# Performance work log

Hardware: AMD Instinct MI355X
Metric: run time of the kernel (lower is better)

Reference implementation:

```python
import jax, jax.numpy as jnp
import numpy as np

EMBED_DIM = 1024
B, S = 4, 2048

def setup_inputs() -> dict:
    key = jax.random.key(0)
    ks = jax.random.split(key, 9)
    D = EMBED_DIM
    scale = 1.0 / np.sqrt(D)
    scale2 = 1.0 / np.sqrt(2 * D)
    return {
        "classical_state": jax.random.normal(ks[0], (B, S, D), jnp.float32),
        "quantum_state": jax.random.normal(ks[1], (B, S, D), jnp.float32),
        "Wc": jax.random.uniform(ks[2], (D, D), jnp.float32, -scale, scale),
        "bc": jax.random.uniform(ks[3], (D,), jnp.float32, -scale, scale),
        "Wq": jax.random.uniform(ks[4], (D, D), jnp.float32, -scale, scale),
        "bq": jax.random.uniform(ks[5], (D,), jnp.float32, -scale, scale),
        "Wg": jax.random.uniform(ks[6], (D, 2 * D), jnp.float32, -scale2, scale2),
        "bg": jax.random.uniform(ks[7], (D,), jnp.float32, -scale2, scale2),
        "temperature": jnp.array(1.0, jnp.float32),
    }

def reference(classical_state, quantum_state, Wc, bc, Wq, bq, Wg, bg, temperature):
    D = classical_state.shape[-1]
    c_proj = jnp.einsum('bsd,ed->bse', classical_state, Wc) + bc  # [B,S,D]
    q_proj = jnp.einsum('bsd,ed->bse', quantum_state, Wq) + bq    # [B,S,D]
    combined = jnp.concatenate([c_proj, q_proj], axis=-1)         # [B,S,2D]
    interface_state = jax.nn.sigmoid(jnp.einsum('bsf,ef->bse', combined, Wg) + bg)
    similarity = jnp.einsum('bsd,btd->bst', c_proj, q_proj) / jnp.sqrt(jnp.asarray(D, c_proj.dtype))
    attention_weights = jax.nn.softmax(similarity / temperature, axis=-1)  # [B,S,S]
    transfer_state = jnp.einsum('bst,btd->bsd', attention_weights, quantum_state)
    return classical_state + interface_state * transfer_state
```

## Files before the change

kernel.cpp:

```cpp
#include <hip/hip_runtime.h>


typedef unsigned short u16;
typedef unsigned char u8;
typedef __bf16 bf16x8 __attribute__((ext_vector_type(8)));
typedef float f32x4 __attribute__((ext_vector_type(4)));

__device__ __forceinline__ u16 f2bf(float f) {
    unsigned int x;
    __builtin_memcpy(&x, &f, 4);
    unsigned int r = x + 0x7FFFu + ((x >> 16) & 1u);
    return (u16)(r >> 16);
}
__device__ __forceinline__ float bf2f(u16 u) {
    unsigned int x = ((unsigned int)u) << 16;
    float f;
    __builtin_memcpy(&f, &x, 4);
    return f;
}
__device__ __forceinline__ u8 f2fp8(float f) {
    int p = __builtin_amdgcn_cvt_pk_fp8_f32(f, f, 0, false);
    return (u8)(p & 0xFF);
}

__device__ __forceinline__ void xcd_tile(int& tx, int& ty) {
    const int gx = gridDim.x;
    const int nwg = gx * gridDim.y;
    const int l = blockIdx.x + gx * blockIdx.y;
    const int per = nwg >> 3;
    const int swz = (l & 7) * per + (l >> 3);
    tx = swz % gx;
    ty = swz / gx;
}

#define GLOBAL_TO_LDS16(gp, lp)                                                           \
    __builtin_amdgcn_global_load_lds((const __attribute__((address_space(1))) void*)(gp), \
                                     (__attribute__((address_space(3))) void*)(lp), 16, 0, 0)

__global__ __launch_bounds__(256, 2) void gemm_proj(
    const u16* __restrict__ Ac, const u16* __restrict__ Aq, int lda,
    const u16* __restrict__ Bp, long sBz, int ldb,
    u8* __restrict__ C8, long sCz, int ldc, int K,
    const float* __restrict__ bc, const float* __restrict__ bq) {
    __shared__ __align__(16) u16 As[2][128 * 64];
    __shared__ __align__(16) u16 Bs[2][128 * 64];

    const int tid  = threadIdx.x;
    const int lane = tid & 63;
    const int wave = tid >> 6;
    const int z    = blockIdx.z;

    const u16* a = z ? Aq : Ac;
    const u16* b = Bp + (long)z * sBz;
    const float* bias = z ? bq : bc;

    int tx, ty;
    xcd_tile(tx, ty);
    const int tileM = ty * 128;
    const int tileN = tx * 128;

    const int wm  = wave >> 1;
    const int wn  = wave & 1;
    const int r16 = lane & 15;
    const int kg  = lane >> 4;

    const int srow = lane >> 3;
    const int sgc  = ((lane & 7) ^ (lane >> 3)) * 8;
    const int swb  = r16 & 7;

    auto stage = [&](int buf, int t) {
        const int k0 = t * 64;
#pragma unroll
        for (int p = 0; p < 4; p++) {
            const int rbase = p * 32 + wave * 8;
            GLOBAL_TO_LDS16(a + (long)(tileM + rbase + srow) * lda + k0 + sgc, &As[buf][rbase * 64]);
            GLOBAL_TO_LDS16(b + (long)(tileN + rbase + srow) * ldb + k0 + sgc, &Bs[buf][rbase * 64]);
        }
    };

    f32x4 acc[4][4] = {};

    const int nt = K / 64;
    stage(0, 0);
    stage(1, 1);

    for (int t = 0; t < nt; t++) {
        const int cur = t & 1;
        if (t + 1 < nt) asm volatile("s_waitcnt vmcnt(8)" ::: "memory");
        else            asm volatile("s_waitcnt vmcnt(0)" ::: "memory");
        __builtin_amdgcn_s_barrier();
        asm volatile("" ::: "memory");

        bf16x8 af[2][4], bfr[2][4];
#pragma unroll
        for (int h = 0; h < 2; h++) {
#pragma unroll
            for (int i = 0; i < 4; i++) {
                const int Ra = wm * 64 + i * 16 + r16;
                af[h][i]  = *(const bf16x8*)&As[cur][Ra * 64 + (((h * 4 + kg) ^ swb)) * 8];
                const int Rb = wn * 64 + i * 16 + r16;
                bfr[h][i] = *(const bf16x8*)&Bs[cur][Rb * 64 + (((h * 4 + kg) ^ swb)) * 8];
            }
        }
#pragma unroll
        for (int h = 0; h < 2; h++)
#pragma unroll
            for (int i = 0; i < 4; i++)
#pragma unroll
                for (int j = 0; j < 4; j++)
                    acc[i][j] = __builtin_amdgcn_mfma_f32_16x16x32_bf16(
                        af[h][i], bfr[h][j], acc[i][j], 0, 0, 0);

        asm volatile("" ::: "memory");
        __builtin_amdgcn_s_barrier();
        if (t + 2 < nt) stage(cur, t + 2);
    }

#pragma unroll
    for (int i = 0; i < 4; i++)
#pragma unroll
        for (int j = 0; j < 4; j++) {
            int col = tileN + wn * 64 + j * 16 + r16;
            float bv = bias[col];
#pragma unroll
            for (int v = 0; v < 4; v++) {
                int row = tileM + wm * 64 + i * 16 + kg * 4 + v;
                C8[(long)z * sCz + (long)row * ldc + col] = f2fp8(acc[i][j][v] + bv);
            }
        }
}

template <int MODE>
__global__ __launch_bounds__(256, 2) void gemm8(
    const u8* __restrict__ A0, const u8* __restrict__ A1, long sAz, int lda, int kSplit,
    const u8* __restrict__ Bp, long sBz, int ldb,
    void* __restrict__ Cp, long cOff, long sCz, int ldc, int K,
    const float* __restrict__ bias, const float* __restrict__ temp,
    const float* __restrict__ cls, const u16* __restrict__ g16,
    float* __restrict__ lsum, long lSz) {
    __shared__ __align__(16) u8 As[2][128 * 128];
    __shared__ __align__(16) u8 Bs[2][128 * 128];

    const int tid  = threadIdx.x;
    const int lane = tid & 63;
    const int wave = tid >> 6;
    const int z    = blockIdx.z;

    const u8* a = A0 + (long)z * sAz;
    const u8* b = Bp + (long)z * sBz;

    int tx, ty;
    xcd_tile(tx, ty);
    const int tileM = ty * 128;
    const int tileN = tx * 128;

    const int wm  = wave >> 1;
    const int wn  = wave & 1;
    const int r16 = lane & 15;
    const int kg  = lane >> 4;

    const int srow = lane >> 3;
    const int sgc  = ((lane & 7) ^ (lane >> 3)) * 16;

    auto stage = [&](int buf, int t) {
        const int k0 = t * 128;
        const u8* Ap = a;
        int kA = k0;
        if (MODE == 1 && k0 >= kSplit) { Ap = A1; kA = k0 - kSplit; }
#pragma unroll
        for (int p = 0; p < 4; p++) {
            const int rbase = p * 32 + wave * 8;
            GLOBAL_TO_LDS16(Ap + (long)(tileM + rbase + srow) * lda + kA + sgc, &As[buf][rbase * 128]);
            GLOBAL_TO_LDS16(b + (long)(tileN + rbase + srow) * ldb + k0 + sgc, &Bs[buf][rbase * 128]);
        }
    };

    f32x4 acc[4][4] = {};

    const int nt = K / 128;
    stage(0, 0);
    stage(1, 1);

    for (int t = 0; t < nt; t++) {
        const int cur = t & 1;
        if (t + 1 < nt) asm volatile("s_waitcnt vmcnt(8)" ::: "memory");
        else            asm volatile("s_waitcnt vmcnt(0)" ::: "memory");
        __builtin_amdgcn_s_barrier();
        asm volatile("" ::: "memory");

#pragma unroll
        for (int h = 0; h < 4; h++) {
            long af[4], bfr[4];
#pragma unroll
            for (int i = 0; i < 4; i++) {
                const int Ra = wm * 64 + i * 16 + r16;
                af[i]  = *(const long*)&As[cur][Ra * 128 + (((h * 2 + (kg >> 1)) ^ (Ra & 7))) * 16 + (kg & 1) * 8];
                const int Rb = wn * 64 + i * 16 + r16;
                bfr[i] = *(const long*)&Bs[cur][Rb * 128 + (((h * 2 + (kg >> 1)) ^ (Rb & 7))) * 16 + (kg & 1) * 8];
            }
#pragma unroll
            for (int i = 0; i < 4; i++)
#pragma unroll
                for (int j = 0; j < 4; j++)
                    acc[i][j] = __builtin_amdgcn_mfma_f32_16x16x32_fp8_fp8(
                        af[i], bfr[j], acc[i][j], 0, 0, 0);
        }

        asm volatile("" ::: "memory");
        __builtin_amdgcn_s_barrier();
        if (t + 2 < nt) stage(cur, t + 2);
    }

    float scale = 1.0f;
    if (MODE == 2) scale = 1.0f / (32.0f * temp[0]);

    u16*   C16 = (u16*)Cp;
    u8*    C8  = (u8*)Cp;
    float* C32 = (float*)Cp;

#pragma unroll
    for (int i = 0; i < 4; i++) {
        float rs[4] = {0.f, 0.f, 0.f, 0.f};
#pragma unroll
        for (int j = 0; j < 4; j++) {
            int col = tileN + wn * 64 + j * 16 + r16;
            float bv = (MODE == 1) ? bias[col] : 0.0f;
#pragma unroll
            for (int v = 0; v < 4; v++) {
                int row = tileM + wm * 64 + i * 16 + kg * 4 + v;
                long idx = cOff + (long)z * sCz + (long)row * ldc + col;
                float val = acc[i][j][v];
                if (MODE == 1) {
                    C16[idx] = f2bf(1.0f / (1.0f + __expf(-(val + bv))));
                } else if (MODE == 2) {
                    float e = __expf(val * scale);
                    C8[idx] = f2fp8(e);
                    rs[v] += e;
                } else {
                    float inv = 1.0f / lsum[(long)z * lSz + row];
                    C32[idx] = cls[idx] + bf2f(g16[idx]) * (val * inv);
                }
            }
        }
        if (MODE == 2) {
#pragma unroll
            for (int v = 0; v < 4; v++) {
                float s = rs[v];
#pragma unroll
                for (int off = 1; off < 16; off <<= 1) s += __shfl_xor(s, off, 64);
                if (r16 == 0) {
                    int row = tileM + wm * 64 + i * 16 + kg * 4 + v;
                    atomicAdd(&lsum[(long)z * lSz + row], s);
                }
            }
        }
    }
}

__global__ __launch_bounds__(256) void prep(
    const f32x4* __restrict__ cls, const f32x4* __restrict__ qnt,
    const f32x4* __restrict__ Wc, const f32x4* __restrict__ Wq, const f32x4* __restrict__ Wg,
    ushort4* __restrict__ clsB, ushort4* __restrict__ qntB,
    ushort4* __restrict__ WcB, ushort4* __restrict__ WqB, unsigned int* __restrict__ Wg8,
    f32x4* __restrict__ l, long nM, long nW, long nG, long nL) {
    long i = (long)blockIdx.x * 256 + threadIdx.x;
    long stride = (long)gridDim.x * 256;
    long total = 2 * nM + 2 * nW + nG + nL;
    for (; i < total; i += stride) {
        if (i < 2 * nM) {
            long j = (i < nM) ? i : i - nM;
            f32x4 v = (i < nM) ? cls[j] : qnt[j];
            ushort4 o;
            o.x = f2bf(v.x); o.y = f2bf(v.y); o.z = f2bf(v.z); o.w = f2bf(v.w);
            if (i < nM) clsB[j] = o; else qntB[j] = o;
        } else if (i < 2 * nM + 2 * nW) {
            long j = i - 2 * nM;
            long k = (j < nW) ? j : j - nW;
            f32x4 v = (j < nW) ? Wc[k] : Wq[k];
            ushort4 o;
            o.x = f2bf(v.x); o.y = f2bf(v.y); o.z = f2bf(v.z); o.w = f2bf(v.w);
            if (j < nW) WcB[k] = o; else WqB[k] = o;
        } else if (i < 2 * nM + 2 * nW + nG) {
            long j = i - 2 * nM - 2 * nW;
            f32x4 v = Wg[j];
            int w = __builtin_amdgcn_cvt_pk_fp8_f32(v.x, v.y, 0, false);
            w = __builtin_amdgcn_cvt_pk_fp8_f32(v.z, v.w, w, true);
            Wg8[j] = (unsigned int)w;
        } else {
            l[i - 2 * nM - 2 * nW - nG] = (f32x4){0.f, 0.f, 0.f, 0.f};
        }
    }
}

__global__ __launch_bounds__(256) void transpose_fp8(const u16* __restrict__ Q,
                                                     u8* __restrict__ QT, int S, int D) {
    __shared__ u8 tile[64][65];
    int bz = blockIdx.z;
    const u16* q = Q + (long)bz * S * D;
    u8* qt = QT + (long)bz * S * D;
    int t0 = blockIdx.x * 64;
    int d0 = blockIdx.y * 64;
    int c = threadIdx.x & 63;
    int r = threadIdx.x >> 6;
#pragma unroll
    for (int i = 0; i < 16; i++) {
        int tl = r + 4 * i;
        tile[tl][c] = f2fp8(bf2f(q[(long)(t0 + tl) * D + d0 + c]));
    }
    __syncthreads();
#pragma unroll
    for (int i = 0; i < 16; i++) {
        int dl = r + 4 * i;
        qt[(long)(d0 + dl) * S + t0 + c] = tile[c][dl];
    }
}

extern "C" void kernel_launch(void* const* d_in, const int* in_sizes, int n_in,
                              void* d_out, int out_size, void* d_ws, size_t ws_size,
                              hipStream_t stream) {
    (void)in_sizes; (void)n_in; (void)out_size;

    const float* classical = (const float*)d_in[0];
    const float* quantum   = (const float*)d_in[1];
    const float* Wc        = (const float*)d_in[2];
    const float* bc        = (const float*)d_in[3];
    const float* Wq        = (const float*)d_in[4];
    const float* bq        = (const float*)d_in[5];
    const float* Wg        = (const float*)d_in[6];
    const float* bg        = (const float*)d_in[7];
    const float* temp      = (const float*)d_in[8];
    float* out = (float*)d_out;

    const int B = 4, S = 2048, D = 1024;
    const long MD = (long)B * S * D;

    float* l    = (float*)d_ws;
    u16* Wc_b   = (u16*)(l + (long)B * S);
    u16* Wq_b   = Wc_b + (long)D * D;
    u8*  Wg8    = (u8*)(Wq_b + (long)D * D);
    u16* cls_b  = (u16*)(Wg8 + (long)D * 2 * D);
    u16* qnt_b  = cls_b + MD;
    u8*  cp8    = (u8*)(qnt_b + MD);
    u8*  qp8    = cp8 + MD;
    u8*  qT8    = qp8 + MD;
    u8*  P8     = qT8 + MD;
    u16* g      = cls_b;

    const size_t fixed_bytes = (size_t)B * S * 4 + 2 * (size_t)D * D * 2 +
        (size_t)D * 2 * D + 2 * (size_t)MD * 2 + 3 * (size_t)MD;
    int CH = 128;
    for (int c = 2048; c >= 128; c >>= 1) {
        if (ws_size >= fixed_bytes + (size_t)B * c * S) { CH = c; break; }
    }

    dim3 blk(256);

    prep<<<2048, blk, 0, stream>>>(
        (const f32x4*)classical, (const f32x4*)quantum,
        (const f32x4*)Wc, (const f32x4*)Wq, (const f32x4*)Wg,
        (ushort4*)cls_b, (ushort4*)qnt_b,
        (ushort4*)Wc_b, (ushort4*)Wq_b, (unsigned int*)Wg8,
        (f32x4*)l, MD / 4, (long)D * D / 4, (long)D * 2 * D / 4, (long)B * S / 4);

    gemm_proj<<<dim3(D / 128, (B * S) / 128, 2), blk, 0, stream>>>(
        cls_b, qnt_b, D, Wc_b, (long)D * D, D, cp8, MD, D, D, bc, bq);

    gemm8<1><<<dim3(D / 128, (B * S) / 128, 1), blk, 0, stream>>>(
        cp8, qp8, 0, D, D, Wg8, 0, 2 * D, g, 0, 0, D, 2 * D,
        bg, nullptr, nullptr, nullptr, nullptr, 0);

    transpose_fp8<<<dim3(S / 64, D / 64, B), blk, 0, stream>>>(qnt_b, qT8, S, D);

    for (int m0 = 0; m0 < S; m0 += CH) {
        gemm8<2><<<dim3(S / 128, CH / 128, B), blk, 0, stream>>>(
            cp8 + (long)m0 * D, nullptr, (long)S * D, D, 1 << 30,
            qp8, (long)S * D, D, P8, 0, (long)CH * S, S, D,
            nullptr, temp, nullptr, nullptr, l + m0, S);
        gemm8<4><<<dim3(D / 128, CH / 128, B), blk, 0, stream>>>(
            P8, nullptr, (long)CH * S, S, 1 << 30, qT8, (long)D * S, S,
            out, (long)m0 * D, (long)S * D, D, S,
            nullptr, nullptr, classical, g, l + m0, S);
    }
}
```

Measured before the change: 281.5 us.

## Use 16x16x128 scaled fp8 MFMA and drop LDS double buffering

```diff
diff --git a/kernel.cpp b/kernel.cpp
--- a/kernel.cpp
+++ b/kernel.cpp
@@ -5,6 +5,8 @@
 typedef unsigned char u8;
 typedef __bf16 bf16x8 __attribute__((ext_vector_type(8)));
 typedef float f32x4 __attribute__((ext_vector_type(4)));
+typedef int i32x4 __attribute__((ext_vector_type(4)));
+typedef int i32x8 __attribute__((ext_vector_type(8)));
 
 __device__ __forceinline__ u16 f2bf(float f) {
     unsigned int x;
@@ -138,8 +140,8 @@
     const float* __restrict__ bias, const float* __restrict__ temp,
     const float* __restrict__ cls, const u16* __restrict__ g16,
     float* __restrict__ lsum, long lSz) {
-    __shared__ __align__(16) u8 As[2][128 * 128];
-    __shared__ __align__(16) u8 Bs[2][128 * 128];
+    __shared__ __align__(16) u8 As[128 * 128];
+    __shared__ __align__(16) u8 Bs[128 * 128];
 
     const int tid  = threadIdx.x;
     const int lane = tid & 63;
@@ -162,53 +164,43 @@
     const int srow = lane >> 3;
     const int sgc  = ((lane & 7) ^ (lane >> 3)) * 16;
 
-    auto stage = [&](int buf, int t) {
-        const int k0 = t * 128;
+    f32x4 acc[4][4] = {};
+
+    for (int k0 = 0; k0 < K; k0 += 128) {
         const u8* Ap = a;
         int kA = k0;
         if (MODE == 1 && k0 >= kSplit) { Ap = A1; kA = k0 - kSplit; }
+
 #pragma unroll
         for (int p = 0; p < 4; p++) {
             const int rbase = p * 32 + wave * 8;
-            GLOBAL_TO_LDS16(Ap + (long)(tileM + rbase + srow) * lda + kA + sgc, &As[buf][rbase * 128]);
-            GLOBAL_TO_LDS16(b + (long)(tileN + rbase + srow) * ldb + k0 + sgc, &Bs[buf][rbase * 128]);
-        }
-    };
-
-    f32x4 acc[4][4] = {};
-
-    const int nt = K / 128;
-    stage(0, 0);
-    stage(1, 1);
-
-    for (int t = 0; t < nt; t++) {
-        const int cur = t & 1;
-        if (t + 1 < nt) asm volatile("s_waitcnt vmcnt(8)" ::: "memory");
-        else            asm volatile("s_waitcnt vmcnt(0)" ::: "memory");
-        __builtin_amdgcn_s_barrier();
-        asm volatile("" ::: "memory");
-
-#pragma unroll
-        for (int h = 0; h < 4; h++) {
-            long af[4], bfr[4];
-#pragma unroll
-            for (int i = 0; i < 4; i++) {
-                const int Ra = wm * 64 + i * 16 + r16;
-                af[i]  = *(const long*)&As[cur][Ra * 128 + (((h * 2 + (kg >> 1)) ^ (Ra & 7))) * 16 + (kg & 1) * 8];
-                const int Rb = wn * 64 + i * 16 + r16;
-                bfr[i] = *(const long*)&Bs[cur][Rb * 128 + (((h * 2 + (kg >> 1)) ^ (Rb & 7))) * 16 + (kg & 1) * 8];
-            }
+            GLOBAL_TO_LDS16(Ap + (long)(tileM + rbase + srow) * lda + kA + sgc, &As[rbase * 128]);
+            GLOBAL_TO_LDS16(b + (long)(tileN + rbase + srow) * ldb + k0 + sgc, &Bs[rbase * 128]);
+        }
+        __syncthreads();
+
+        i32x8 af[4];
+#pragma unroll
+        for (int i = 0; i < 4; i++) {
+            const int Ra = wm * 64 + i * 16 + r16;
+            const u8* base = &As[Ra * 128];
+            i32x4 lo = *(const i32x4*)&base[(((2 * kg)     ^ (Ra & 7))) * 16];
+            i32x4 hi = *(const i32x4*)&base[(((2 * kg + 1) ^ (Ra & 7))) * 16];
+            af[i] = __builtin_shufflevector(lo, hi, 0, 1, 2, 3, 4, 5, 6, 7);
+        }
+#pragma unroll
+        for (int j = 0; j < 4; j++) {
+            const int Rb = wn * 64 + j * 16 + r16;
+            const u8* base = &Bs[Rb * 128];
+            i32x4 lo = *(const i32x4*)&base[(((2 * kg)     ^ (Rb & 7))) * 16];
+            i32x4 hi = *(const i32x4*)&base[(((2 * kg + 1) ^ (Rb & 7))) * 16];
+            i32x8 bfr = __builtin_shufflevector(lo, hi, 0, 1, 2, 3, 4, 5, 6, 7);
 #pragma unroll
             for (int i = 0; i < 4; i++)
-#pragma unroll
-                for (int j = 0; j < 4; j++)
-                    acc[i][j] = __builtin_amdgcn_mfma_f32_16x16x32_fp8_fp8(
-                        af[i], bfr[j], acc[i][j], 0, 0, 0);
-        }
-
-        asm volatile("" ::: "memory");
-        __builtin_amdgcn_s_barrier();
-        if (t + 2 < nt) stage(cur, t + 2);
+                acc[i][j] = __builtin_amdgcn_mfma_scale_f32_16x16x128_f8f6f4(
+                    af[i], bfr, acc[i][j], 0, 0, 0, 127, 0, 127);
+        }
+        __syncthreads();
     }
 
     float scale = 1.0f;
```

After: 266.5 us. 5.3% less time.
